# Kernel tuning notes

Measured on AMD Instinct MI355X. Metric: run time of the kernel, lower is better.

The kernel has to match this reference:

```python
import jax, jax.numpy as jnp
import numpy as np

B, P, N, H = 2, 512, 8, 32
INIT_RANGE = 0.02


def setup_inputs() -> dict:
    key = jax.random.key(0)
    k1, k2, k3 = jax.random.split(key, 3)
    d = jax.random.normal(k1, (B, P, N, H), dtype=jnp.float32)
    e = jax.random.normal(k2, (B, P, N, H), dtype=jnp.float32)
    W = jax.random.normal(k3, (N, H, H, H), dtype=jnp.float32) * INIT_RANGE
    return {"d": d, "e": e, "W": W}


def reference(d, e, W):
    # Trilinear contraction: v[b,p1,p2,n,h3] = sum_{h1,h2} d[b,p1,n,h1] e[b,p2,n,h2] W[n,h1,h2,h3]
    # Decompose into two batched matmuls to avoid the naive 4-way product:
    # tmp[b,p1,n,h2,h3] = sum_h1 d[b,p1,n,h1] W[n,h1,h2,h3]
    tmp = jnp.einsum('bpni,nijk->bpnjk', d, W)
    # v[b,p1,p2,n,h3] = sum_h2 tmp[b,p1,n,h2,h3] e[b,p2,n,h2]
    v = jnp.einsum('bpnjk,bqnj->bpqnk', tmp, e)
    return v
```

## Files before the change

kernel.cpp:

```cpp
#include <hip/hip_runtime.h>

#define BB 2
#define PP 512
#define NN 8
#define HH 32

typedef float f4     __attribute__((ext_vector_type(4)));
typedef float f32x4  __attribute__((ext_vector_type(4)));
typedef short bf16x8 __attribute__((ext_vector_type(8)));

__device__ __forceinline__ short f2bf(float f) {
  union { float f; unsigned u; } v; v.f = f;
  unsigned r = v.u + 0x7FFFu + ((v.u >> 16) & 1u);
  return (short)(r >> 16);
}

__global__ __launch_bounds__(256) void wtrans_kernel(
    const float* __restrict__ W, float* __restrict__ WT) {
  const int blk = blockIdx.x;
  const int t   = threadIdx.x;
  __shared__ float ls[32][33];
  const float* src = W  + (size_t)blk * 1024;
  float*       dst = WT + (size_t)blk * 1024;
  #pragma unroll
  for (int r = 0; r < 4; ++r) {
    const int h2 = r * 8 + (t >> 5), h3 = t & 31;
    ls[h2][h3] = src[h2 * 32 + h3];
  }
  __syncthreads();
  #pragma unroll
  for (int r = 0; r < 4; ++r) {
    const int h3 = r * 8 + (t >> 5), h2 = t & 31;
    dst[h3 * 32 + h2] = ls[h2][h3];
  }
}

__global__ __launch_bounds__(256) void prep2_kernel(
    const float* __restrict__ d, const float* __restrict__ WT,
    const float* __restrict__ e, short* __restrict__ tmpT,
    short* __restrict__ eB) {
  const int bid = blockIdx.x;
  const int t   = threadIdx.x;

  if (bid >= 512) {
    const int i = ((bid - 512) * 256 + t) * 8;
    const f4 e0 = *(const f4*)(e + i);
    const f4 e1 = *(const f4*)(e + i + 4);
    bf16x8 v;
    v[0] = f2bf(e0[0]); v[1] = f2bf(e0[1]); v[2] = f2bf(e0[2]); v[3] = f2bf(e0[3]);
    v[4] = f2bf(e1[0]); v[5] = f2bf(e1[1]); v[6] = f2bf(e1[2]); v[7] = f2bf(e1[3]);
    *(bf16x8*)(eB + i) = v;
    return;
  }

  const int b      = bid >> 8;
  const int rem    = bid & 255;
  const int npair  = rem >> 6;
  const int p1base = (rem & 63) * 8;

  __shared__ float dsh[2][32][8];
  {
    const int h1 = t & 31, p1l = (t >> 5) & 7;
    #pragma unroll
    for (int r = 0; r < 2; ++r)
      dsh[r][h1][p1l] =
          d[(size_t)((b * PP + p1base + p1l) * NN + npair * 2 + r) * HH + h1];
  }
  __syncthreads();

  const int np  = t >> 7;
  const int h3  = (t >> 2) & 31;
  const int h2g = t & 3;
  const int n   = npair * 2 + np;

  float acc[8][8];
  #pragma unroll
  for (int p = 0; p < 8; ++p)
    #pragma unroll
    for (int q = 0; q < 8; ++q) acc[p][q] = 0.f;

  const float* wb = WT + ((size_t)(n * HH) * HH + h3) * HH + h2g * 8;
  for (int h1 = 0; h1 < 32; ++h1) {
    const f4 w0 = *(const f4*)(wb + (size_t)h1 * 1024);
    const f4 w1 = *(const f4*)(wb + (size_t)h1 * 1024 + 4);
    const f4 d0 = *(const f4*)&dsh[np][h1][0];
    const f4 d1 = *(const f4*)&dsh[np][h1][4];
    #pragma unroll
    for (int p = 0; p < 4; ++p) {
      #pragma unroll
      for (int q = 0; q < 4; ++q) {
        acc[p][q]         = fmaf(d0[p], w0[q], acc[p][q]);
        acc[p][q + 4]     = fmaf(d0[p], w1[q], acc[p][q + 4]);
        acc[p + 4][q]     = fmaf(d1[p], w0[q], acc[p + 4][q]);
        acc[p + 4][q + 4] = fmaf(d1[p], w1[q], acc[p + 4][q + 4]);
      }
    }
  }

  const size_t obase =
      ((size_t)(b * PP + p1base) * NN + n) * (HH * HH) + h3 * 32 + h2g * 8;
  #pragma unroll
  for (int p = 0; p < 8; ++p) {
    bf16x8 v;
    #pragma unroll
    for (int q = 0; q < 8; ++q) v[q] = f2bf(acc[p][q]);
    *(bf16x8*)(tmpT + obase + (size_t)p * (NN * HH * HH)) = v;
  }
}

__global__ __launch_bounds__(256, 4) void vmain_kernel(
    const short* __restrict__ eB, const short* __restrict__ tmpT,
    float* __restrict__ out) {
  const int bid = blockIdx.x;
  const int b   = bid >> 9;
  const int p1  = bid & 511;
  const int t   = threadIdx.x;
  const int wv  = t >> 6;
  const int l   = t & 63;
  const int lr  = l & 15;
  const int lk  = l >> 4;

  __shared__ float lbuf[4][16][128];
  float* wl = &lbuf[wv][0][0];

  bf16x8 bfr[8][2];
  const short* tb = tmpT + (size_t)(b * PP + p1) * (NN * HH * HH);
  #pragma unroll
  for (int n = 0; n < 8; ++n)
    #pragma unroll
    for (int c = 0; c < 2; ++c)
      bfr[n][c] = __builtin_nontemporal_load(
          (const bf16x8*)(tb + n * (HH * HH) + (c * 16 + lr) * 32 + lk * 8));

  const short* ebb  = eB + (size_t)b * (PP * NN * HH);
  float*       outb = out + (size_t)(b * PP + p1) * (PP * NN * HH);
  const f32x4  z    = {0.f, 0.f, 0.f, 0.f};

  for (int i = 0; i < 8; ++i) {
    const int m0 = (wv * 8 + i) * 16;
    #pragma unroll
    for (int half = 0; half < 2; ++half) {
      const int n0 = half * 4;
      #pragma unroll
      for (int nn = 0; nn < 4; ++nn) {
        const int n = n0 + nn;
        const bf16x8 a =
            *(const bf16x8*)(ebb + (size_t)((m0 + lr) * NN + n) * HH + lk * 8);
        const f32x4 c0 = __builtin_amdgcn_mfma_f32_16x16x32_bf16(bfr[n][0], a, z, 0, 0, 0);
        const f32x4 c1 = __builtin_amdgcn_mfma_f32_16x16x32_bf16(bfr[n][1], a, z, 0, 0, 0);
        const int s0 = (nn * 8 + lk)     ^ (lr & 7);
        const int s1 = (nn * 8 + 4 + lk) ^ (lr & 7);
        *(f32x4*)(wl + lr * 128 + s0 * 4) = c0;
        *(f32x4*)(wl + lr * 128 + s1 * 4) = c1;
      }
      #pragma unroll
      for (int j = 0; j < 8; ++j) {
        const int row  = 2 * j + (l >> 5);
        const int slot = l & 31;
        const f32x4 v = *(const f32x4*)(wl + row * 128 + ((slot ^ (row & 7)) * 4));
        __builtin_nontemporal_store(
            v, (f32x4*)(outb + (size_t)(m0 + row) * (NN * HH) + n0 * HH + slot * 4));
      }
    }
  }
}

__global__ __launch_bounds__(256, 4) void fused_kernel(
    const float* __restrict__ d, const float* __restrict__ e,
    const float* __restrict__ W, float* __restrict__ out) {
  const int bid = blockIdx.x;
  const int b   = bid >> 9;
  const int p1  = bid & 511;
  const int t   = threadIdx.x;

  __shared__ float dsh[NN * HH];
  __shared__ short tsh[NN * HH * HH];
  dsh[t] = d[(size_t)(b * PP + p1) * (NN * HH) + t];
  __syncthreads();

  const int h3  = t & 31;
  const int h2b = t >> 5;
  for (int n = 0; n < 8; ++n) {
    f4 dv[8];
    #pragma unroll
    for (int j = 0; j < 8; ++j) dv[j] = *(const f4*)&dsh[n * 32 + j * 4];
    const float* Wn = W + (size_t)n * (HH * HH * HH);
    #pragma unroll
    for (int h2s = 0; h2s < 4; ++h2s) {
      const int h2 = h2s * 8 + h2b;
      float acc = 0.f;
      #pragma unroll
      for (int j = 0; j < 8; ++j)
        #pragma unroll
        for (int k = 0; k < 4; ++k)
          acc = fmaf(dv[j][k], Wn[(j * 4 + k) * 1024 + h2 * 32 + h3], acc);
      tsh[n * 1024 + h3 * 32 + h2] = f2bf(acc);
    }
  }
  __syncthreads();

  const int wv = t >> 6;
  const int l  = t & 63;
  const int lr = l & 15;
  const int lk = l >> 4;
  bf16x8 bfr[8][2];
  #pragma unroll
  for (int n = 0; n < 8; ++n)
    #pragma unroll
    for (int c = 0; c < 2; ++c)
      bfr[n][c] = *(const bf16x8*)&tsh[n * (HH * HH) + (c * 16 + lr) * 32 + lk * 8];

  const float* eb   = e + (size_t)b * (PP * NN * HH);
  float*       outb = out + (size_t)(b * PP + p1) * (PP * NN * HH);
  const f32x4  z    = {0.f, 0.f, 0.f, 0.f};
  for (int i = 0; i < 8; ++i) {
    const int m0 = (wv * 8 + i) * 16;
    #pragma unroll
    for (int n = 0; n < 8; ++n) {
      const float* ep = eb + (size_t)(((m0 + lr) * NN + n) * HH + lk * 8);
      const f4 e0 = *(const f4*)ep;
      const f4 e1 = *(const f4*)(ep + 4);
      bf16x8 a;
      a[0] = f2bf(e0[0]); a[1] = f2bf(e0[1]); a[2] = f2bf(e0[2]); a[3] = f2bf(e0[3]);
      a[4] = f2bf(e1[0]); a[5] = f2bf(e1[1]); a[6] = f2bf(e1[2]); a[7] = f2bf(e1[3]);
      const f32x4 c0 = __builtin_amdgcn_mfma_f32_16x16x32_bf16(bfr[n][0], a, z, 0, 0, 0);
      const f32x4 c1 = __builtin_amdgcn_mfma_f32_16x16x32_bf16(bfr[n][1], a, z, 0, 0, 0);
      float* op = outb + (size_t)(m0 + lr) * (NN * HH) + n * HH + lk * 4;
      *(f32x4*)op        = c0;
      *(f32x4*)(op + 16) = c1;
    }
  }
}

extern "C" void kernel_launch(void* const* d_in, const int* in_sizes, int n_in,
                              void* d_out, int out_size, void* d_ws, size_t ws_size,
                              hipStream_t stream) {
  const float* d = (const float*)d_in[0];
  const float* e = (const float*)d_in[1];
  const float* W = (const float*)d_in[2];
  float* out = (float*)d_out;

  const size_t tmp_bytes = (size_t)BB * PP * NN * HH * HH * sizeof(short);
  const size_t eb_bytes  = (size_t)BB * PP * NN * HH * sizeof(short);
  const size_t wt_bytes  = (size_t)NN * HH * HH * HH * sizeof(float);
  if (ws_size >= tmp_bytes + eb_bytes + wt_bytes) {
    short* tmpT = (short*)d_ws;
    short* eB   = (short*)((char*)d_ws + tmp_bytes);
    float* WT   = (float*)((char*)d_ws + tmp_bytes + eb_bytes);
    wtrans_kernel<<<dim3(NN * HH), dim3(256), 0, stream>>>(W, WT);
    prep2_kernel<<<dim3(512 + 128), dim3(256), 0, stream>>>(d, WT, e, tmpT, eB);
    vmain_kernel<<<dim3(BB * PP), dim3(256), 0, stream>>>(eB, tmpT, out);
  } else {
    fused_kernel<<<dim3(BB * PP), dim3(256), 0, stream>>>(d, e, W, out);
  }
}
```

Before: 137.3 us.

## Drop W transpose kernel, pre-swizzle e into MFMA fragment order, use cached stores

Removes the separate W transpose launch. The prep kernel now reads W directly with strided scalar loads (coalesced across h3 lanes) instead of float4 loads from a transposed copy. The e-to-bf16 conversion now writes e in MFMA fragment order, so each lane in the main kernel loads one contiguous 16-byte chunk per tile. Nontemporal loads and stores are also replaced with ordinary ones. This saves a launch and a pass over W, but the prep inner loop issues more load instructions, and the change in cache policy on the large output write could help or hurt.

```diff
diff --git a/kernel.cpp b/kernel.cpp
--- a/kernel.cpp
+++ b/kernel.cpp
@@ -15,41 +15,27 @@
   return (short)(r >> 16);
 }
 
-__global__ __launch_bounds__(256) void wtrans_kernel(
-    const float* __restrict__ W, float* __restrict__ WT) {
-  const int blk = blockIdx.x;
-  const int t   = threadIdx.x;
-  __shared__ float ls[32][33];
-  const float* src = W  + (size_t)blk * 1024;
-  float*       dst = WT + (size_t)blk * 1024;
-  #pragma unroll
-  for (int r = 0; r < 4; ++r) {
-    const int h2 = r * 8 + (t >> 5), h3 = t & 31;
-    ls[h2][h3] = src[h2 * 32 + h3];
-  }
-  __syncthreads();
-  #pragma unroll
-  for (int r = 0; r < 4; ++r) {
-    const int h3 = r * 8 + (t >> 5), h2 = t & 31;
-    dst[h3 * 32 + h2] = ls[h2][h3];
-  }
-}
-
-__global__ __launch_bounds__(256) void prep2_kernel(
-    const float* __restrict__ d, const float* __restrict__ WT,
+__global__ __launch_bounds__(256) void prep_all_kernel(
+    const float* __restrict__ d, const float* __restrict__ W,
     const float* __restrict__ e, short* __restrict__ tmpT,
-    short* __restrict__ eB) {
+    short* __restrict__ eBf) {
   const int bid = blockIdx.x;
   const int t   = threadIdx.x;
 
   if (bid >= 512) {
-    const int i = ((bid - 512) * 256 + t) * 8;
-    const f4 e0 = *(const f4*)(e + i);
-    const f4 e1 = *(const f4*)(e + i + 4);
+    const int ft = (bid - 512) * 256 + t;
+    const int l  = ft & 63;
+    const int n  = (ft >> 6) & 7;
+    const int pt = (ft >> 9) & 31;
+    const int b  = ft >> 14;
+    const float* src =
+        e + (((size_t)(b * PP + pt * 16 + (l & 15)) * NN + n) * HH + (l >> 4) * 8);
+    const f4 e0 = *(const f4*)src;
+    const f4 e1 = *(const f4*)(src + 4);
     bf16x8 v;
     v[0] = f2bf(e0[0]); v[1] = f2bf(e0[1]); v[2] = f2bf(e0[2]); v[3] = f2bf(e0[3]);
     v[4] = f2bf(e1[0]); v[5] = f2bf(e1[1]); v[6] = f2bf(e1[2]); v[7] = f2bf(e1[3]);
-    *(bf16x8*)(eB + i) = v;
+    *(bf16x8*)(eBf + (size_t)ft * 8) = v;
     return;
   }
 
@@ -79,20 +65,22 @@
     #pragma unroll
     for (int q = 0; q < 8; ++q) acc[p][q] = 0.f;
 
-  const float* wb = WT + ((size_t)(n * HH) * HH + h3) * HH + h2g * 8;
+  const float* wb = W + (size_t)n * 32768 + h2g * 8 * 32 + h3;
   for (int h1 = 0; h1 < 32; ++h1) {
-    const f4 w0 = *(const f4*)(wb + (size_t)h1 * 1024);
-    const f4 w1 = *(const f4*)(wb + (size_t)h1 * 1024 + 4);
+    const float* wr = wb + (size_t)h1 * 1024;
+    float wq[8];
+    #pragma unroll
+    for (int q = 0; q < 8; ++q) wq[q] = wr[q * 32];
     const f4 d0 = *(const f4*)&dsh[np][h1][0];
     const f4 d1 = *(const f4*)&dsh[np][h1][4];
     #pragma unroll
     for (int p = 0; p < 4; ++p) {
       #pragma unroll
       for (int q = 0; q < 4; ++q) {
-        acc[p][q]         = fmaf(d0[p], w0[q], acc[p][q]);
-        acc[p][q + 4]     = fmaf(d0[p], w1[q], acc[p][q + 4]);
-        acc[p + 4][q]     = fmaf(d1[p], w0[q], acc[p + 4][q]);
-        acc[p + 4][q + 4] = fmaf(d1[p], w1[q], acc[p + 4][q + 4]);
+        acc[p][q]         = fmaf(d0[p], wq[q],     acc[p][q]);
+        acc[p][q + 4]     = fmaf(d0[p], wq[q + 4], acc[p][q + 4]);
+        acc[p + 4][q]     = fmaf(d1[p], wq[q],     acc[p + 4][q]);
+        acc[p + 4][q + 4] = fmaf(d1[p], wq[q + 4], acc[p + 4][q + 4]);
       }
     }
   }
@@ -109,7 +97,7 @@
 }
 
 __global__ __launch_bounds__(256, 4) void vmain_kernel(
-    const short* __restrict__ eB, const short* __restrict__ tmpT,
+    const short* __restrict__ eBf, const short* __restrict__ tmpT,
     float* __restrict__ out) {
   const int bid = blockIdx.x;
   const int b   = bid >> 9;
@@ -129,15 +117,15 @@
   for (int n = 0; n < 8; ++n)
     #pragma unroll
     for (int c = 0; c < 2; ++c)
-      bfr[n][c] = __builtin_nontemporal_load(
-          (const bf16x8*)(tb + n * (HH * HH) + (c * 16 + lr) * 32 + lk * 8));
-
-  const short* ebb  = eB + (size_t)b * (PP * NN * HH);
+      bfr[n][c] = *(const bf16x8*)(tb + n * (HH * HH) + (c * 16 + lr) * 32 + lk * 8);
+
+  const short* eb   = eBf + (size_t)b * (32 * NN * 512);
   float*       outb = out + (size_t)(b * PP + p1) * (PP * NN * HH);
   const f32x4  z    = {0.f, 0.f, 0.f, 0.f};
 
   for (int i = 0; i < 8; ++i) {
-    const int m0 = (wv * 8 + i) * 16;
+    const int pt = wv * 8 + i;
+    const int m0 = pt * 16;
     #pragma unroll
     for (int half = 0; half < 2; ++half) {
       const int n0 = half * 4;
@@ -145,7 +133,7 @@
       for (int nn = 0; nn < 4; ++nn) {
         const int n = n0 + nn;
         const bf16x8 a =
-            *(const bf16x8*)(ebb + (size_t)((m0 + lr) * NN + n) * HH + lk * 8);
+            *(const bf16x8*)(eb + (((size_t)(pt * NN + n)) << 9) + l * 8);
         const f32x4 c0 = __builtin_amdgcn_mfma_f32_16x16x32_bf16(bfr[n][0], a, z, 0, 0, 0);
         const f32x4 c1 = __builtin_amdgcn_mfma_f32_16x16x32_bf16(bfr[n][1], a, z, 0, 0, 0);
         const int s0 = (nn * 8 + lk)     ^ (lr & 7);
@@ -158,8 +146,7 @@
         const int row  = 2 * j + (l >> 5);
         const int slot = l & 31;
         const f32x4 v = *(const f32x4*)(wl + row * 128 + ((slot ^ (row & 7)) * 4));
-        __builtin_nontemporal_store(
-            v, (f32x4*)(outb + (size_t)(m0 + row) * (NN * HH) + n0 * HH + slot * 4));
+        *(f32x4*)(outb + (size_t)(m0 + row) * (NN * HH) + n0 * HH + slot * 4) = v;
       }
     }
   }
@@ -242,14 +229,11 @@
 
   const size_t tmp_bytes = (size_t)BB * PP * NN * HH * HH * sizeof(short);
   const size_t eb_bytes  = (size_t)BB * PP * NN * HH * sizeof(short);
-  const size_t wt_bytes  = (size_t)NN * HH * HH * HH * sizeof(float);
-  if (ws_size >= tmp_bytes + eb_bytes + wt_bytes) {
+  if (ws_size >= tmp_bytes + eb_bytes) {
     short* tmpT = (short*)d_ws;
-    short* eB   = (short*)((char*)d_ws + tmp_bytes);
-    float* WT   = (float*)((char*)d_ws + tmp_bytes + eb_bytes);
-    wtrans_kernel<<<dim3(NN * HH), dim3(256), 0, stream>>>(W, WT);
-    prep2_kernel<<<dim3(512 + 128), dim3(256), 0, stream>>>(d, WT, e, tmpT, eB);
-    vmain_kernel<<<dim3(BB * PP), dim3(256), 0, stream>>>(eB, tmpT, out);
+    short* eBf  = (short*)((char*)d_ws + tmp_bytes);
+    prep_all_kernel<<<dim3(512 + 128), dim3(256), 0, stream>>>(d, W, e, tmpT, eBf);
+    vmain_kernel<<<dim3(BB * PP), dim3(256), 0, stream>>>(eBf, tmpT, out);
   } else {
     fused_kernel<<<dim3(BB * PP), dim3(256), 0, stream>>>(d, e, W, out);
   }
```

After: 132.3 us. 1.04x faster.
